# Kernel tuning notes

Hardware: AMD Instinct MI355X
Metric: run time of the kernel (lower is better)

The kernel has to match this reference:

```python
import jax, jax.numpy as jnp
import numpy as np

B, C, N, K = 2, 128, 8192, 16
DL = 128  # dim_L; Fourier half-dim = 64; mlp hidden = 32


def setup_inputs() -> dict:
    key = jax.random.key(0)
    ks = jax.random.split(key, 16)
    s = 0.05
    return {
        "x": jax.random.normal(ks[0], (B, C, N, 1), jnp.float32),
        "coords": jax.random.normal(ks[1], (B, N, 4), jnp.float32),
        "idx": jax.random.randint(ks[2], (B, N, K), 0, N, jnp.int64),
        "B_gauss": jax.random.normal(ks[3], (4, DL // 2), jnp.float32),
        "W1": jax.random.normal(ks[4], (DL, DL // 4), jnp.float32) * s,
        "b1": jax.random.normal(ks[5], (DL // 4,), jnp.float32) * s,
        "W2": jax.random.normal(ks[6], (DL // 4, C), jnp.float32) * s,
        "b2": jax.random.normal(ks[7], (C,), jnp.float32) * s,
        "Wq": jax.random.normal(ks[8], (C, C), jnp.float32) * s,
        "bq": jax.random.normal(ks[9], (C,), jnp.float32) * s,
        "Wk": jax.random.normal(ks[10], (C, C), jnp.float32) * s,
        "bk": jax.random.normal(ks[11], (C,), jnp.float32) * s,
        "Wv": jax.random.normal(ks[12], (C, C), jnp.float32) * s,
        "bv": jax.random.normal(ks[13], (C,), jnp.float32) * s,
        "Wo": jax.random.normal(ks[14], (C, C), jnp.float32) * s,
        "bo": jax.random.normal(ks[15], (C,), jnp.float32) * s,
    }


def reference(x, coords, idx, B_gauss, W1, b1, W2, b2, Wq, bq, Wk, bk, Wv, bv, Wo, bo):
    xs = x[..., 0]  # [B, C, N]
    # gather neighbor coords/features via KNN idx (vmapped over batch)
    nb_coords = jax.vmap(lambda c, i: c[i])(coords, idx)          # [B, N, K, 4]
    nb_feats = jax.vmap(lambda f, i: f[:, i])(xs, idx)            # [B, C, N, K]
    delta_p = nb_coords - coords[:, :, None, :]                   # [B, N, K, 4]
    # random-Fourier geometric embedding
    proj = jnp.matmul(delta_p, B_gauss)                           # [B, N, K, DL/2]
    two_pi = 2.0 * jnp.pi
    E_freq = jnp.concatenate([jnp.sin(two_pi * proj), jnp.cos(two_pi * proj)], axis=-1)
    h = jax.nn.relu(E_freq @ W1 + b1) @ W2 + b2                   # [B, N, K, C]
    E_geo = jnp.transpose(h, (0, 3, 1, 2))                        # [B, C, N, K]
    # 1x1 conv projections == channel matmuls (PyTorch conv weight acts as out<-in)
    Q = jnp.einsum('oc,bcn->bon', Wq, xs) + bq[None, :, None]     # [B, C, N]
    KV_in = nb_feats + E_geo                                      # [B, C, N, K]
    Kt = jnp.einsum('oc,bcnk->bonk', Wk, KV_in) + bk[None, :, None, None]
    Vt = jnp.einsum('oc,bcnk->bonk', Wv, KV_in) + bv[None, :, None, None]
    # local dot-product attention over K neighbors
    attn = jnp.sum(Q[..., None] * Kt, axis=1, keepdims=True) / jnp.sqrt(jnp.float32(C))
    attn = jax.nn.softmax(attn, axis=-1)                          # [B, 1, N, K]
    out = jnp.sum(attn * Vt, axis=-1, keepdims=True)              # [B, C, N, 1]
    out = jnp.einsum('oc,bcnk->bonk', Wo, out) + bo[None, :, None, None]
    return out
```

## Files before the change

kernel.cpp:

```cpp
#include <hip/hip_runtime.h>


using u16 = unsigned short;
using u32 = unsigned int;
using u64 = unsigned long long;

typedef short bf16x8 __attribute__((ext_vector_type(8)));
typedef float f32x4  __attribute__((ext_vector_type(4)));

__device__ __forceinline__ float bl(u32 u) { return __uint_as_float(u << 16); }
__device__ __forceinline__ float bh(u32 u) { return __uint_as_float(u & 0xffff0000u); }
__device__ __forceinline__ float b2f(u16 u) { return __uint_as_float(((u32)u) << 16); }
__device__ __forceinline__ u16 f2b(float f) {
    u32 u = __float_as_uint(f);
    u32 r = u + 0x7fffu + ((u >> 16) & 1u);
    return (u16)(r >> 16);
}
__device__ __forceinline__ float dot8(uint4 wv, const float* xp) {
    float4 a = *(const float4*)xp;
    float4 b = *(const float4*)(xp + 4);
    return bl(wv.x)*a.x + bh(wv.x)*a.y + bl(wv.y)*a.z + bh(wv.y)*a.w
         + bl(wv.z)*b.x + bh(wv.z)*b.y + bl(wv.w)*b.z + bh(wv.w)*b.w;
}
__device__ __forceinline__ u64 pack4(float a, float b, float c, float d) {
    return (u64)f2b(a) | ((u64)f2b(b) << 16) | ((u64)f2b(c) << 32) | ((u64)f2b(d) << 48);
}

__device__ __forceinline__ int fidxA(int m, int c) {
    return (((m >> 4)*4 + (c >> 5))*64 + ((c >> 3) & 3)*16 + (m & 15))*8 + (c & 7);
}

__global__ void __launch_bounds__(512)
k_prep(const float* __restrict__ Wq, const float* __restrict__ bq,
       const float* __restrict__ Wk, const float* __restrict__ bk,
       const float* __restrict__ Wv, const float* __restrict__ bv,
       const float* __restrict__ Wo, const float* __restrict__ bo,
       const float* __restrict__ W1, const float* __restrict__ W2,
       u16* __restrict__ Afrag, u16* __restrict__ Wovfrag,
       u16* __restrict__ W1frag, u16* __restrict__ W2frag,
       u16* __restrict__ W2Tfrag,
       float* __restrict__ bA, float* __restrict__ su,
       float* __restrict__ bov, float* __restrict__ d0)
{
    const int blk = blockIdx.x, tid = threadIdx.x;
    const int i = tid & 127, p = tid >> 7;

    if (blk < 128) {
        __shared__ float sWk[128], sWo[128];
        __shared__ float s_pA[4][128], s_pV[4][128];
        if (tid < 128) sWk[tid] = Wk[tid*128 + blk];
        else if (tid < 256) sWo[tid-128] = Wo[blk*128 + (tid-128)];
        __syncthreads();
        float accA = 0.f, accV = 0.f;
        #pragma unroll 8
        for (int o = p*32; o < p*32 + 32; ++o) {
            accA += sWk[o] * Wq[o*128 + i];
            accV += sWo[o] * Wv[o*128 + i];
        }
        s_pA[p][i] = accA; s_pV[p][i] = accV;
        __syncthreads();
        if (tid < 128) {
            float v = s_pA[0][tid] + s_pA[1][tid] + s_pA[2][tid] + s_pA[3][tid];
            Afrag[fidxA(blk, tid)] = f2b(v);
        } else if (tid < 256) {
            int ii = tid - 128;
            float v = s_pV[0][ii] + s_pV[1][ii] + s_pV[2][ii] + s_pV[3][ii];
            Wovfrag[fidxA(blk, ii)] = f2b(v);
        }
    } else if (blk == 128) {
        __shared__ float s_r[3][4][128];
        float a1 = 0.f, a2 = 0.f, a3 = 0.f;
        #pragma unroll 8
        for (int o = p*32; o < p*32 + 32; ++o) {
            a1 += Wk[o*128 + i] * bq[o];
            a2 += Wq[o*128 + i] * bk[o];
            a3 += Wo[i*128 + o] * bv[o];
        }
        s_r[0][p][i] = a1; s_r[1][p][i] = a2; s_r[2][p][i] = a3;
        __syncthreads();
        if (tid < 128) {
            bA[tid] = s_r[0][0][tid] + s_r[0][1][tid] + s_r[0][2][tid] + s_r[0][3][tid];
        } else if (tid < 256) {
            int ii = tid - 128;
            su[ii] = s_r[1][0][ii] + s_r[1][1][ii] + s_r[1][2][ii] + s_r[1][3][ii];
        } else if (tid < 384) {
            int ii = tid - 256;
            bov[ii] = s_r[2][0][ii] + s_r[2][1][ii] + s_r[2][2][ii] + s_r[2][3][ii] + bo[ii];
        } else if (tid < 448) {
            int l = tid - 384;
            float part = bq[l]*bk[l] + bq[l+64]*bk[l+64];
            part += __shfl_xor(part, 1);
            part += __shfl_xor(part, 2);
            part += __shfl_xor(part, 4);
            part += __shfl_xor(part, 8);
            part += __shfl_xor(part, 16);
            part += __shfl_xor(part, 32);
            if (l == 0) *d0 = part;
        }
    } else {
        for (int e = tid; e < 4096; e += 512) {
            int ii = e & 127, r2 = e >> 7;
            {
                int nt = r2 >> 4, lmm = r2 & 15;
                int ks = ii >> 5, q = (ii >> 3) & 3, j = ii & 7;
                W1frag[((nt*4 + ks)*64 + q*16 + lmm)*8 + j] = f2b(W1[ii*32 + r2]);
            }
            {
                int mt = r2 >> 4, lmm = r2 & 15;
                int ks = ii >> 5, q = (ii >> 3) & 3, j = ii & 7;
                W2frag[((mt*4 + ks)*64 + q*16 + lmm)*8 + j] = f2b(W2[r2*128 + ii]);
            }
            {
                int mt = ii >> 4, lmm = ii & 15;
                int q = r2 >> 3, j = r2 & 7;
                W2Tfrag[(mt*64 + q*16 + lmm)*8 + j] = f2b(W2[r2*128 + ii]);
            }
        }
    }
}

__global__ void k_tr(const float* __restrict__ x, u16* __restrict__ xT)
{
    __shared__ u16 tile[32][33];
    const int blk = blockIdx.x;
    const int b  = blk >> 10;
    const int ct = (blk >> 8) & 3;
    const int nt = blk & 255;
    const int tx = threadIdx.x & 31, ty = threadIdx.x >> 5;
    const size_t xb = (size_t)b * 128 * 8192;
    #pragma unroll
    for (int j = 0; j < 4; ++j) {
        int c = ct*32 + ty + j*8;
        tile[ty + j*8][tx] = f2b(x[xb + (size_t)c * 8192 + (size_t)(nt*32 + tx)]);
    }
    __syncthreads();
    #pragma unroll
    for (int j = 0; j < 4; ++j) {
        int n = nt*32 + ty + j*8;
        xT[xb + (size_t)n * 128 + (size_t)(ct*32 + tx)] = tile[tx][ty + j*8];
    }
}

__global__ void __launch_bounds__(512)
k_main(const u16* __restrict__ xT, const float* __restrict__ coords,
       const int* __restrict__ idx, const float* __restrict__ Bg,
       const float* __restrict__ b1g, const float* __restrict__ b2g,
       const u16* __restrict__ Afrag, const u16* __restrict__ Wovfrag,
       const u16* __restrict__ W1frag, const u16* __restrict__ W2frag,
       const u16* __restrict__ W2Tfrag,
       const float* __restrict__ bAg, const float* __restrict__ sug,
       const float* __restrict__ bovg, const float* __restrict__ d0g,
       float* __restrict__ out)
{
    __shared__ __align__(16) u16   buf[256][136];
    __shared__ __align__(16) u16   sH[256][40];
    __shared__ __align__(16) u16   s_qkb[16][136];
    __shared__ __align__(16) u16   s_gb[16][40];
    __shared__ __align__(16) u16   s_wtb[16][136];
    __shared__ __align__(16) float s_xb[16][132];
    __shared__ __align__(16) float s_del[256][4];
    __shared__ float s_sc[16][17];
    __shared__ float s_attn[16][17];
    __shared__ u16   sHbar[32][18];
    __shared__ float s_e0[16];
    __shared__ __align__(16) float s_b2[128], s_su[128];
    __shared__ float s_bA[128], s_bov[128], s_b1[32];
    __shared__ __align__(16) float sBgT[64][4];
    __shared__ int s_idx[256];

    const int tid = threadIdx.x;
    const int w = tid >> 6, l = tid & 63, lm = l & 15, lq = l >> 4;
    const int g0 = blockIdx.x * 16;
    const int bsel = g0 >> 13;
    const int n0 = g0 & 8191;
    const size_t bbase = ((size_t)bsel) << 13;
    const float inv_sqrtC = 0.08838834764831845f;

    if (tid < 128) {
        s_bA[tid] = bAg[tid]; s_su[tid] = sug[tid];
        s_bov[tid] = bovg[tid]; s_b2[tid] = b2g[tid];
    } else if (tid < 160) {
        s_b1[tid-128] = b1g[tid-128];
    } else if (tid >= 256) {
        int q = tid - 256;
        sBgT[q >> 2][q & 3] = Bg[(q & 3)*64 + (q >> 2)];
    }
    const float c_d0 = *d0g;

    if (tid < 256) {
        int j = idx[(size_t)g0*16 + tid];
        s_idx[tid] = j;
        float4 cj = *(const float4*)&coords[(size_t)(bbase + j)*4];
        float4 cn = *(const float4*)&coords[(size_t)(g0 + (tid >> 4))*4];
        *(float4*)s_del[tid] = make_float4(cj.x-cn.x, cj.y-cn.y, cj.z-cn.z, cj.w-cn.w);
    }
    f32x4 accq = {0.f, 0.f, 0.f, 0.f};
    {
        const bf16x8* Af = (const bf16x8*)Afrag;
        #pragma unroll
        for (int ks = 0; ks < 4; ++ks) {
            bf16x8 a = Af[(w*4 + ks)*64 + l];
            bf16x8 bfr = *(const bf16x8*)&xT[(((size_t)(g0 + lm)) << 7) + ks*32 + lq*8];
            accq = __builtin_amdgcn_mfma_f32_16x16x32_bf16(a, bfr, accq, 0, 0, 0);
        }
    }
    __syncthreads();

    {
        int c0 = w*16 + lq*4;
        *(u64*)&s_qkb[lm][c0] = pack4(accq[0] + s_bA[c0],   accq[1] + s_bA[c0+1],
                                      accq[2] + s_bA[c0+2], accq[3] + s_bA[c0+3]);
    }
    __syncthreads();

    {
        const int row = tid >> 1, ch0 = (tid & 1)*8;
        const size_t rbase = ((size_t)(bbase + s_idx[row])) << 7;
        #pragma unroll
        for (int cc = 0; cc < 8; ++cc) {
            int chunk = ch0 + cc;
            *(uint4*)&buf[row][chunk*8] = *(const uint4*)&xT[rbase + chunk*8];
        }
    }
    {
        const bf16x8* W1f = (const bf16x8*)W1frag;
        bf16x8 w1f[2][4];
        #pragma unroll
        for (int nt = 0; nt < 2; ++nt)
            #pragma unroll
            for (int ks = 0; ks < 4; ++ks) w1f[nt][ks] = W1f[(nt*4 + ks)*64 + l];
        float4 bgc[2][8];
        #pragma unroll
        for (int ksp = 0; ksp < 2; ++ksp)
            #pragma unroll
            for (int j = 0; j < 8; ++j)
                bgc[ksp][j] = *(const float4*)sBgT[ksp*32 + lq*8 + j];
        #pragma unroll
        for (int mi = 0; mi < 2; ++mi) {
            const int mt = w*2 + mi;
            float4 d = *(const float4*)s_del[mt*16 + lm];
            bf16x8 ea[4];
            #pragma unroll
            for (int ksp = 0; ksp < 2; ++ksp) {
                #pragma unroll
                for (int jp = 0; jp < 4; ++jp) {
                    float4 ga = bgc[ksp][jp*2], gb = bgc[ksp][jp*2+1];
                    float p0 = d.x*ga.x + d.y*ga.y + d.z*ga.z + d.w*ga.w;
                    float p1 = d.x*gb.x + d.y*gb.y + d.z*gb.z + d.w*gb.w;
                    p0 -= floorf(p0); p1 -= floorf(p1);
                    ((u32*)&ea[ksp])[jp]   = (u32)f2b(__builtin_amdgcn_sinf(p0))
                                           | ((u32)f2b(__builtin_amdgcn_sinf(p1)) << 16);
                    ((u32*)&ea[ksp+2])[jp] = (u32)f2b(__builtin_amdgcn_cosf(p0))
                                           | ((u32)f2b(__builtin_amdgcn_cosf(p1)) << 16);
                }
            }
            f32x4 acch[2] = {{0.f,0.f,0.f,0.f},{0.f,0.f,0.f,0.f}};
            #pragma unroll
            for (int ks = 0; ks < 4; ++ks) {
                acch[0] = __builtin_amdgcn_mfma_f32_16x16x32_bf16(ea[ks], w1f[0][ks], acch[0], 0,0,0);
                acch[1] = __builtin_amdgcn_mfma_f32_16x16x32_bf16(ea[ks], w1f[1][ks], acch[1], 0,0,0);
            }
            #pragma unroll
            for (int nt = 0; nt < 2; ++nt) {
                float b1v = s_b1[nt*16 + lm];
                #pragma unroll
                for (int r = 0; r < 4; ++r)
                    sH[mt*16 + lq*4 + r][nt*16 + lm] = f2b(fmaxf(acch[nt][r] + b1v, 0.f));
            }
        }
    }
    if (w < 2) {
        const bf16x8* W2f = (const bf16x8*)W2frag;
        f32x4 accg = {0.f,0.f,0.f,0.f};
        #pragma unroll
        for (int ks = 0; ks < 4; ++ks) {
            bf16x8 a = W2f[(w*4 + ks)*64 + l];
            bf16x8 bv = *(const bf16x8*)&s_qkb[lm][ks*32 + lq*8];
            accg = __builtin_amdgcn_mfma_f32_16x16x32_bf16(a, bv, accg, 0, 0, 0);
        }
        int m0 = w*16 + lq*4;
        *(u64*)&s_gb[lm][m0] = pack4(accg[0], accg[1], accg[2], accg[3]);
    } else if (w < 4) {
        int t = tid - 128, n = t >> 3, sub = t & 7, c0 = sub*16;
        uint4 q0 = *(const uint4*)&s_qkb[n][c0];
        uint4 q1 = *(const uint4*)&s_qkb[n][c0+8];
        uint4 x0 = *(const uint4*)&xT[(((size_t)(g0 + n)) << 7) + c0];
        uint4 x1 = *(const uint4*)&xT[(((size_t)(g0 + n)) << 7) + c0 + 8];
        float part = dot8(q0, &s_b2[c0]) + dot8(q1, &s_b2[c0+8])
                   + dot8(x0, &s_su[c0]) + dot8(x1, &s_su[c0+8]);
        part += __shfl_xor(part, 1);
        part += __shfl_xor(part, 2);
        part += __shfl_xor(part, 4);
        if (sub == 0) s_e0[n] = part + c_d0;
    }
    __syncthreads();

    {
        bf16x8 bq4[5];
        #pragma unroll
        for (int ks = 0; ks < 4; ++ks) bq4[ks] = *(const bf16x8*)&s_qkb[lm][ks*32 + lq*8];
        bq4[4] = *(const bf16x8*)&s_gb[lm][lq*8];
        #pragma unroll
        for (int mi = 0; mi < 2; ++mi) {
            const int mt = w*2 + mi;
            f32x4 acc = {0.f,0.f,0.f,0.f};
            #pragma unroll
            for (int ks = 0; ks < 4; ++ks) {
                bf16x8 a = *(const bf16x8*)&buf[mt*16 + lm][ks*32 + lq*8];
                acc = __builtin_amdgcn_mfma_f32_16x16x32_bf16(a, bq4[ks], acc, 0, 0, 0);
            }
            {
                bf16x8 a = *(const bf16x8*)&sH[mt*16 + lm][lq*8];
                acc = __builtin_amdgcn_mfma_f32_16x16x32_bf16(a, bq4[4], acc, 0, 0, 0);
            }
            if (lm == mt) {
                #pragma unroll
                for (int r = 0; r < 4; ++r) s_sc[mt][lq*4 + r] = acc[r];
            }
        }
    }
    __syncthreads();

    if (tid < 256) {
        int n = tid >> 4, k = tid & 15;
        float s = (s_sc[n][k] + s_e0[n]) * inv_sqrtC;
        float mx = s;
        mx = fmaxf(mx, __shfl_xor(mx, 1, 16));
        mx = fmaxf(mx, __shfl_xor(mx, 2, 16));
        mx = fmaxf(mx, __shfl_xor(mx, 4, 16));
        mx = fmaxf(mx, __shfl_xor(mx, 8, 16));
        float ex = __expf(s - mx);
        float sm = ex;
        sm += __shfl_xor(sm, 1, 16);
        sm += __shfl_xor(sm, 2, 16);
        sm += __shfl_xor(sm, 4, 16);
        sm += __shfl_xor(sm, 8, 16);
        s_attn[n][k] = ex / sm;
    }
    __syncthreads();

    {
        int n = tid >> 5, cs = tid & 31, c0 = cs*4;
        float a0[16];
        #pragma unroll
        for (int k = 0; k < 16; ++k) a0[k] = s_attn[n][k];
        float4 facc = *(const float4*)&s_b2[c0];
        #pragma unroll
        for (int k = 0; k < 16; ++k) {
            uint2 v = *(const uint2*)&buf[n*16 + k][c0];
            facc.x += a0[k]*bl(v.x); facc.y += a0[k]*bh(v.x);
            facc.z += a0[k]*bl(v.y); facc.w += a0[k]*bh(v.y);
        }
        *(float4*)&s_xb[n][c0] = facc;
        int m = tid & 31;
        float hacc = 0.f;
        #pragma unroll
        for (int k = 0; k < 16; ++k) hacc += a0[k] * b2f(sH[n*16 + k][m]);
        sHbar[m][n] = f2b(hacc);
    }
    __syncthreads();

    {
        const bf16x8* W2Tf = (const bf16x8*)W2Tfrag;
        bf16x8 a = W2Tf[w*64 + l];
        bf16x8 bv;
        #pragma unroll
        for (int j = 0; j < 8; ++j) bv[j] = (short)sHbar[lq*8 + j][lm];
        f32x4 accw = {0.f,0.f,0.f,0.f};
        accw = __builtin_amdgcn_mfma_f32_16x16x32_bf16(a, bv, accw, 0, 0, 0);
        int c0 = w*16 + lq*4;
        float4 xb4 = *(const float4*)&s_xb[lm][c0];
        *(u64*)&s_wtb[lm][c0] = pack4(xb4.x + accw[0], xb4.y + accw[1],
                                      xb4.z + accw[2], xb4.w + accw[3]);
    }
    __syncthreads();

    {
        const bf16x8* Wvf = (const bf16x8*)Wovfrag;
        f32x4 acco = {0.f,0.f,0.f,0.f};
        #pragma unroll
        for (int ks = 0; ks < 4; ++ks) {
            bf16x8 a = Wvf[(w*4 + ks)*64 + l];
            bf16x8 bv = *(const bf16x8*)&s_wtb[lm][ks*32 + lq*8];
            acco = __builtin_amdgcn_mfma_f32_16x16x32_bf16(a, bv, acco, 0, 0, 0);
        }
        #pragma unroll
        for (int r = 0; r < 4; ++r) {
            int o = w*16 + lq*4 + r;
            out[(((size_t)(bsel*128 + o)) << 13) + n0 + lm] = acco[r] + s_bov[o];
        }
    }
}

extern "C" void kernel_launch(void* const* d_in, const int* in_sizes, int n_in,
                              void* d_out, int out_size, void* d_ws, size_t ws_size,
                              hipStream_t stream)
{
    const float* x      = (const float*)d_in[0];
    const float* coords = (const float*)d_in[1];
    const int*   idx    = (const int*)d_in[2];
    const float* Bg     = (const float*)d_in[3];
    const float* W1     = (const float*)d_in[4];
    const float* b1     = (const float*)d_in[5];
    const float* W2     = (const float*)d_in[6];
    const float* b2     = (const float*)d_in[7];
    const float* Wq     = (const float*)d_in[8];
    const float* bq     = (const float*)d_in[9];
    const float* Wk     = (const float*)d_in[10];
    const float* bk     = (const float*)d_in[11];
    const float* Wv     = (const float*)d_in[12];
    const float* bv     = (const float*)d_in[13];
    const float* Wo     = (const float*)d_in[14];
    const float* bo     = (const float*)d_in[15];
    float* out = (float*)d_out;

    char* ws = (char*)d_ws;
    u16*   Afrag   = (u16*)(ws);
    u16*   Wovfrag = (u16*)(ws + 32768);
    u16*   W1frag  = (u16*)(ws + 65536);
    u16*   W2frag  = (u16*)(ws + 73728);
    u16*   W2Tfrag = (u16*)(ws + 81920);
    float* bA      = (float*)(ws + 90112);
    float* su      = (float*)(ws + 90624);
    float* bov     = (float*)(ws + 91136);
    float* d0      = (float*)(ws + 91648);
    u16*   xT      = (u16*)(ws + 94208);

    k_prep<<<130, 512, 0, stream>>>(Wq, bq, Wk, bk, Wv, bv, Wo, bo, W1, W2,
                                    Afrag, Wovfrag, W1frag, W2frag, W2Tfrag,
                                    bA, su, bov, d0);
    k_tr<<<2048, 256, 0, stream>>>(x, xT);
    k_main<<<1024, 512, 0, stream>>>(xT, coords, idx, Bg, b1, b2,
                                     Afrag, Wovfrag, W1frag, W2frag, W2Tfrag,
                                     bA, su, bov, d0, out);
}
```

Before: 137.1 us.

## Halve main-kernel tile, drop neighbor LDS staging, merge prep and transpose kernels

The main kernel now handles 8 points per block with 256 threads instead of 16 points with 512 threads, and uses launch bounds of 5 blocks per CU. This cuts shared memory sharply and should raise occupancy. Gathered neighbor features are no longer staged in the 256x136 LDS buffer but read straight from global xT inside the MFMA and aggregation loops. The weight-prep and transpose kernels are merged into one launch to save a kernel boundary. The trade-off is that half the MFMA lanes (lm>=8) do wasted work, and global gathers are repeated, relying on the cache.

```diff
diff --git a/kernel.cpp b/kernel.cpp
--- a/kernel.cpp
+++ b/kernel.cpp
@@ -25,26 +25,49 @@
 __device__ __forceinline__ u64 pack4(float a, float b, float c, float d) {
     return (u64)f2b(a) | ((u64)f2b(b) << 16) | ((u64)f2b(c) << 32) | ((u64)f2b(d) << 48);
 }
-
 __device__ __forceinline__ int fidxA(int m, int c) {
     return (((m >> 4)*4 + (c >> 5))*64 + ((c >> 3) & 3)*16 + (m & 15))*8 + (c & 7);
 }
 
 __global__ void __launch_bounds__(512)
-k_prep(const float* __restrict__ Wq, const float* __restrict__ bq,
-       const float* __restrict__ Wk, const float* __restrict__ bk,
-       const float* __restrict__ Wv, const float* __restrict__ bv,
-       const float* __restrict__ Wo, const float* __restrict__ bo,
-       const float* __restrict__ W1, const float* __restrict__ W2,
-       u16* __restrict__ Afrag, u16* __restrict__ Wovfrag,
-       u16* __restrict__ W1frag, u16* __restrict__ W2frag,
-       u16* __restrict__ W2Tfrag,
-       float* __restrict__ bA, float* __restrict__ su,
-       float* __restrict__ bov, float* __restrict__ d0)
+k_pt(const float* __restrict__ x,
+     const float* __restrict__ Wq, const float* __restrict__ bq,
+     const float* __restrict__ Wk, const float* __restrict__ bk,
+     const float* __restrict__ Wv, const float* __restrict__ bv,
+     const float* __restrict__ Wo, const float* __restrict__ bo,
+     const float* __restrict__ W1, const float* __restrict__ W2,
+     u16* __restrict__ Afrag, u16* __restrict__ Wovfrag,
+     u16* __restrict__ W1frag, u16* __restrict__ W2frag,
+     u16* __restrict__ W2Tfrag,
+     float* __restrict__ bA, float* __restrict__ su,
+     float* __restrict__ bov, float* __restrict__ d0,
+     u16* __restrict__ xT)
 {
     const int blk = blockIdx.x, tid = threadIdx.x;
+
+    if (blk >= 130) {
+        __shared__ u16 tile[32][33];
+        const int blk2 = blk - 130;
+        const int b  = blk2 >> 10;
+        const int ct = (blk2 >> 8) & 3;
+        const int nt = blk2 & 255;
+        const int tx = tid & 31, ty = tid >> 5;
+        const size_t xb = (size_t)b * 128 * 8192;
+        #pragma unroll
+        for (int j = 0; j < 2; ++j) {
+            int c = ct*32 + ty + j*16;
+            tile[ty + j*16][tx] = f2b(x[xb + (size_t)c * 8192 + (size_t)(nt*32 + tx)]);
+        }
+        __syncthreads();
+        #pragma unroll
+        for (int j = 0; j < 2; ++j) {
+            int n = nt*32 + ty + j*16;
+            xT[xb + (size_t)n * 128 + (size_t)(ct*32 + tx)] = tile[tx][ty + j*16];
+        }
+        return;
+    }
+
     const int i = tid & 127, p = tid >> 7;
-
     if (blk < 128) {
         __shared__ float sWk[128], sWo[128];
         __shared__ float s_pA[4][128], s_pV[4][128];
@@ -119,29 +142,7 @@
     }
 }
 
-__global__ void k_tr(const float* __restrict__ x, u16* __restrict__ xT)
-{
-    __shared__ u16 tile[32][33];
-    const int blk = blockIdx.x;
-    const int b  = blk >> 10;
-    const int ct = (blk >> 8) & 3;
-    const int nt = blk & 255;
-    const int tx = threadIdx.x & 31, ty = threadIdx.x >> 5;
-    const size_t xb = (size_t)b * 128 * 8192;
-    #pragma unroll
-    for (int j = 0; j < 4; ++j) {
-        int c = ct*32 + ty + j*8;
-        tile[ty + j*8][tx] = f2b(x[xb + (size_t)c * 8192 + (size_t)(nt*32 + tx)]);
-    }
-    __syncthreads();
-    #pragma unroll
-    for (int j = 0; j < 4; ++j) {
-        int n = nt*32 + ty + j*8;
-        xT[xb + (size_t)n * 128 + (size_t)(ct*32 + tx)] = tile[tx][ty + j*8];
-    }
-}
-
-__global__ void __launch_bounds__(512)
+__global__ void __launch_bounds__(256, 5)
 k_main(const u16* __restrict__ xT, const float* __restrict__ coords,
        const int* __restrict__ idx, const float* __restrict__ Bg,
        const float* __restrict__ b1g, const float* __restrict__ b2g,
@@ -152,25 +153,24 @@
        const float* __restrict__ bovg, const float* __restrict__ d0g,
        float* __restrict__ out)
 {
-    __shared__ __align__(16) u16   buf[256][136];
-    __shared__ __align__(16) u16   sH[256][40];
-    __shared__ __align__(16) u16   s_qkb[16][136];
-    __shared__ __align__(16) u16   s_gb[16][40];
-    __shared__ __align__(16) u16   s_wtb[16][136];
-    __shared__ __align__(16) float s_xb[16][132];
-    __shared__ __align__(16) float s_del[256][4];
-    __shared__ float s_sc[16][17];
-    __shared__ float s_attn[16][17];
-    __shared__ u16   sHbar[32][18];
-    __shared__ float s_e0[16];
+    __shared__ __align__(16) u16   sH[128][40];
+    __shared__ __align__(16) u16   s_qkb[8][136];
+    __shared__ __align__(16) u16   s_gb[8][40];
+    __shared__ __align__(16) u16   s_wtb[8][136];
+    __shared__ __align__(16) float s_xb[8][132];
+    __shared__ __align__(16) float s_del[128][4];
+    __shared__ float s_sc[8][17];
+    __shared__ float s_attn[8][17];
+    __shared__ u16   sHbar[32][12];
+    __shared__ float s_e0[8];
     __shared__ __align__(16) float s_b2[128], s_su[128];
     __shared__ float s_bA[128], s_bov[128], s_b1[32];
     __shared__ __align__(16) float sBgT[64][4];
-    __shared__ int s_idx[256];
+    __shared__ int s_idx[128];
 
     const int tid = threadIdx.x;
-    const int w = tid >> 6, l = tid & 63, lm = l & 15, lq = l >> 4;
-    const int g0 = blockIdx.x * 16;
+    const int w = tid >> 6, l = tid & 63, lm = l & 15, lq = l >> 4, lmm = lm & 7;
+    const int g0 = blockIdx.x * 8;
     const int bsel = g0 >> 13;
     const int n0 = g0 & 8191;
     const size_t bbase = ((size_t)bsel) << 13;
@@ -181,47 +181,46 @@
         s_bov[tid] = bovg[tid]; s_b2[tid] = b2g[tid];
     } else if (tid < 160) {
         s_b1[tid-128] = b1g[tid-128];
-    } else if (tid >= 256) {
-        int q = tid - 256;
-        sBgT[q >> 2][q & 3] = Bg[(q & 3)*64 + (q >> 2)];
-    }
+    }
+    sBgT[tid >> 2][tid & 3] = Bg[(tid & 3)*64 + (tid >> 2)];
     const float c_d0 = *d0g;
 
-    if (tid < 256) {
+    if (tid < 128) {
         int j = idx[(size_t)g0*16 + tid];
         s_idx[tid] = j;
         float4 cj = *(const float4*)&coords[(size_t)(bbase + j)*4];
         float4 cn = *(const float4*)&coords[(size_t)(g0 + (tid >> 4))*4];
         *(float4*)s_del[tid] = make_float4(cj.x-cn.x, cj.y-cn.y, cj.z-cn.z, cj.w-cn.w);
     }
-    f32x4 accq = {0.f, 0.f, 0.f, 0.f};
+    f32x4 accq[2] = {{0.f,0.f,0.f,0.f},{0.f,0.f,0.f,0.f}};
     {
         const bf16x8* Af = (const bf16x8*)Afrag;
-        #pragma unroll
-        for (int ks = 0; ks < 4; ++ks) {
-            bf16x8 a = Af[(w*4 + ks)*64 + l];
-            bf16x8 bfr = *(const bf16x8*)&xT[(((size_t)(g0 + lm)) << 7) + ks*32 + lq*8];
-            accq = __builtin_amdgcn_mfma_f32_16x16x32_bf16(a, bfr, accq, 0, 0, 0);
-        }
-    }
-    __syncthreads();
-
-    {
-        int c0 = w*16 + lq*4;
-        *(u64*)&s_qkb[lm][c0] = pack4(accq[0] + s_bA[c0],   accq[1] + s_bA[c0+1],
-                                      accq[2] + s_bA[c0+2], accq[3] + s_bA[c0+3]);
-    }
-    __syncthreads();
-
-    {
-        const int row = tid >> 1, ch0 = (tid & 1)*8;
-        const size_t rbase = ((size_t)(bbase + s_idx[row])) << 7;
-        #pragma unroll
-        for (int cc = 0; cc < 8; ++cc) {
-            int chunk = ch0 + cc;
-            *(uint4*)&buf[row][chunk*8] = *(const uint4*)&xT[rbase + chunk*8];
-        }
-    }
+        bf16x8 bfr[4];
+        #pragma unroll
+        for (int ks = 0; ks < 4; ++ks)
+            bfr[ks] = *(const bf16x8*)&xT[(((size_t)(g0 + lmm)) << 7) + ks*32 + lq*8];
+        #pragma unroll
+        for (int mi = 0; mi < 2; ++mi) {
+            const int ct = w*2 + mi;
+            #pragma unroll
+            for (int ks = 0; ks < 4; ++ks) {
+                bf16x8 a = Af[(ct*4 + ks)*64 + l];
+                accq[mi] = __builtin_amdgcn_mfma_f32_16x16x32_bf16(a, bfr[ks], accq[mi], 0, 0, 0);
+            }
+        }
+    }
+    __syncthreads();
+
+    if (lm < 8) {
+        #pragma unroll
+        for (int mi = 0; mi < 2; ++mi) {
+            int c0 = (w*2 + mi)*16 + lq*4;
+            *(u64*)&s_qkb[lm][c0] = pack4(accq[mi][0] + s_bA[c0],   accq[mi][1] + s_bA[c0+1],
+                                          accq[mi][2] + s_bA[c0+2], accq[mi][3] + s_bA[c0+3]);
+        }
+    }
+    __syncthreads();
+
     {
         const bf16x8* W1f = (const bf16x8*)W1frag;
         bf16x8 w1f[2][4];
@@ -229,12 +228,6 @@
         for (int nt = 0; nt < 2; ++nt)
             #pragma unroll
             for (int ks = 0; ks < 4; ++ks) w1f[nt][ks] = W1f[(nt*4 + ks)*64 + l];
-        float4 bgc[2][8];
-        #pragma unroll
-        for (int ksp = 0; ksp < 2; ++ksp)
-            #pragma unroll
-            for (int j = 0; j < 8; ++j)
-                bgc[ksp][j] = *(const float4*)sBgT[ksp*32 + lq*8 + j];
         #pragma unroll
         for (int mi = 0; mi < 2; ++mi) {
             const int mt = w*2 + mi;
@@ -244,7 +237,9 @@
             for (int ksp = 0; ksp < 2; ++ksp) {
                 #pragma unroll
                 for (int jp = 0; jp < 4; ++jp) {
-                    float4 ga = bgc[ksp][jp*2], gb = bgc[ksp][jp*2+1];
+                    int f = ksp*32 + lq*8 + jp*2;
+                    float4 ga = *(const float4*)sBgT[f];
+                    float4 gb = *(const float4*)sBgT[f+1];
                     float p0 = d.x*ga.x + d.y*ga.y + d.z*ga.z + d.w*ga.w;
                     float p1 = d.x*gb.x + d.y*gb.y + d.z*gb.z + d.w*gb.w;
                     p0 -= floorf(p0); p1 -= floorf(p1);
@@ -275,38 +270,44 @@
         #pragma unroll
         for (int ks = 0; ks < 4; ++ks) {
             bf16x8 a = W2f[(w*4 + ks)*64 + l];
-            bf16x8 bv = *(const bf16x8*)&s_qkb[lm][ks*32 + lq*8];
+            bf16x8 bv = *(const bf16x8*)&s_qkb[lmm][ks*32 + lq*8];
             accg = __builtin_amdgcn_mfma_f32_16x16x32_bf16(a, bv, accg, 0, 0, 0);
         }
-        int m0 = w*16 + lq*4;
-        *(u64*)&s_gb[lm][m0] = pack4(accg[0], accg[1], accg[2], accg[3]);
-    } else if (w < 4) {
-        int t = tid - 128, n = t >> 3, sub = t & 7, c0 = sub*16;
-        uint4 q0 = *(const uint4*)&s_qkb[n][c0];
-        uint4 q1 = *(const uint4*)&s_qkb[n][c0+8];
-        uint4 x0 = *(const uint4*)&xT[(((size_t)(g0 + n)) << 7) + c0];
-        uint4 x1 = *(const uint4*)&xT[(((size_t)(g0 + n)) << 7) + c0 + 8];
-        float part = dot8(q0, &s_b2[c0]) + dot8(q1, &s_b2[c0+8])
-                   + dot8(x0, &s_su[c0]) + dot8(x1, &s_su[c0+8]);
-        part += __shfl_xor(part, 1);
-        part += __shfl_xor(part, 2);
-        part += __shfl_xor(part, 4);
-        if (sub == 0) s_e0[n] = part + c_d0;
+        if (lm < 8) {
+            int m0 = w*16 + lq*4;
+            *(u64*)&s_gb[lm][m0] = pack4(accg[0], accg[1], accg[2], accg[3]);
+        }
+    } else {
+        int t = tid - 128;
+        if (t < 64) {
+            int n = t >> 3, sub = t & 7, c0 = sub*16;
+            uint4 q0 = *(const uint4*)&s_qkb[n][c0];
+            uint4 q1 = *(const uint4*)&s_qkb[n][c0+8];
+            uint4 x0 = *(const uint4*)&xT[(((size_t)(g0 + n)) << 7) + c0];
+            uint4 x1 = *(const uint4*)&xT[(((size_t)(g0 + n)) << 7) + c0 + 8];
+            float part = dot8(q0, &s_b2[c0]) + dot8(q1, &s_b2[c0+8])
+                       + dot8(x0, &s_su[c0]) + dot8(x1, &s_su[c0+8]);
+            part += __shfl_xor(part, 1);
+            part += __shfl_xor(part, 2);
+            part += __shfl_xor(part, 4);
+            if (sub == 0) s_e0[n] = part + c_d0;
+        }
     }
     __syncthreads();
 
     {
         bf16x8 bq4[5];
         #pragma unroll
-        for (int ks = 0; ks < 4; ++ks) bq4[ks] = *(const bf16x8*)&s_qkb[lm][ks*32 + lq*8];
-        bq4[4] = *(const bf16x8*)&s_gb[lm][lq*8];
+        for (int ks = 0; ks < 4; ++ks) bq4[ks] = *(const bf16x8*)&s_qkb[lmm][ks*32 + lq*8];
+        bq4[4] = *(const bf16x8*)&s_gb[lmm][lq*8];
         #pragma unroll
         for (int mi = 0; mi < 2; ++mi) {
             const int mt = w*2 + mi;
+            const size_t rb = ((size_t)(bbase + s_idx[mt*16 + lm])) << 7;
             f32x4 acc = {0.f,0.f,0.f,0.f};
             #pragma unroll
             for (int ks = 0; ks < 4; ++ks) {
-                bf16x8 a = *(const bf16x8*)&buf[mt*16 + lm][ks*32 + lq*8];
+                bf16x8 a = *(const bf16x8*)&xT[rb + ks*32 + lq*8];
                 acc = __builtin_amdgcn_mfma_f32_16x16x32_bf16(a, bq4[ks], acc, 0, 0, 0);
             }
             {
@@ -321,7 +322,7 @@
     }
     __syncthreads();
 
-    if (tid < 256) {
+    if (tid < 128) {
         int n = tid >> 4, k = tid & 15;
         float s = (s_sc[n][k] + s_e0[n]) * inv_sqrtC;
         float mx = s;
@@ -347,12 +348,12 @@
         float4 facc = *(const float4*)&s_b2[c0];
         #pragma unroll
         for (int k = 0; k < 16; ++k) {
-            uint2 v = *(const uint2*)&buf[n*16 + k][c0];
+            uint2 v = *(const uint2*)&xT[(((size_t)(bbase + s_idx[n*16 + k])) << 7) + c0];
             facc.x += a0[k]*bl(v.x); facc.y += a0[k]*bh(v.x);
             facc.z += a0[k]*bl(v.y); facc.w += a0[k]*bh(v.y);
         }
         *(float4*)&s_xb[n][c0] = facc;
-        int m = tid & 31;
+        int m = cs;
         float hacc = 0.f;
         #pragma unroll
         for (int k = 0; k < 16; ++k) hacc += a0[k] * b2f(sH[n*16 + k][m]);
@@ -362,32 +363,46 @@
 
     {
         const bf16x8* W2Tf = (const bf16x8*)W2Tfrag;
-        bf16x8 a = W2Tf[w*64 + l];
         bf16x8 bv;
         #pragma unroll
-        for (int j = 0; j < 8; ++j) bv[j] = (short)sHbar[lq*8 + j][lm];
-        f32x4 accw = {0.f,0.f,0.f,0.f};
-        accw = __builtin_amdgcn_mfma_f32_16x16x32_bf16(a, bv, accw, 0, 0, 0);
-        int c0 = w*16 + lq*4;
-        float4 xb4 = *(const float4*)&s_xb[lm][c0];
-        *(u64*)&s_wtb[lm][c0] = pack4(xb4.x + accw[0], xb4.y + accw[1],
-                                      xb4.z + accw[2], xb4.w + accw[3]);
+        for (int j = 0; j < 8; ++j) bv[j] = (short)sHbar[lq*8 + j][lmm];
+        #pragma unroll
+        for (int mi = 0; mi < 2; ++mi) {
+            const int mt = w*2 + mi;
+            bf16x8 a = W2Tf[mt*64 + l];
+            f32x4 accw = {0.f,0.f,0.f,0.f};
+            accw = __builtin_amdgcn_mfma_f32_16x16x32_bf16(a, bv, accw, 0, 0, 0);
+            if (lm < 8) {
+                int c0 = mt*16 + lq*4;
+                float4 xb4 = *(const float4*)&s_xb[lm][c0];
+                *(u64*)&s_wtb[lm][c0] = pack4(xb4.x + accw[0], xb4.y + accw[1],
+                                              xb4.z + accw[2], xb4.w + accw[3]);
+            }
+        }
     }
     __syncthreads();
 
     {
         const bf16x8* Wvf = (const bf16x8*)Wovfrag;
-        f32x4 acco = {0.f,0.f,0.f,0.f};
-        #pragma unroll
-        for (int ks = 0; ks < 4; ++ks) {
-            bf16x8 a = Wvf[(w*4 + ks)*64 + l];
-            bf16x8 bv = *(const bf16x8*)&s_wtb[lm][ks*32 + lq*8];
-            acco = __builtin_amdgcn_mfma_f32_16x16x32_bf16(a, bv, acco, 0, 0, 0);
-        }
-        #pragma unroll
-        for (int r = 0; r < 4; ++r) {
-            int o = w*16 + lq*4 + r;
-            out[(((size_t)(bsel*128 + o)) << 13) + n0 + lm] = acco[r] + s_bov[o];
+        bf16x8 bv[4];
+        #pragma unroll
+        for (int ks = 0; ks < 4; ++ks) bv[ks] = *(const bf16x8*)&s_wtb[lmm][ks*32 + lq*8];
+        #pragma unroll
+        for (int mi = 0; mi < 2; ++mi) {
+            const int ct = w*2 + mi;
+            f32x4 acco = {0.f,0.f,0.f,0.f};
+            #pragma unroll
+            for (int ks = 0; ks < 4; ++ks) {
+                bf16x8 a = Wvf[(ct*4 + ks)*64 + l];
+                acco = __builtin_amdgcn_mfma_f32_16x16x32_bf16(a, bv[ks], acco, 0, 0, 0);
+            }
+            if (lm < 8) {
+                #pragma unroll
+                for (int r = 0; r < 4; ++r) {
+                    int o = ct*16 + lq*4 + r;
+                    out[(((size_t)(bsel*128 + o)) << 13) + n0 + lm] = acco[r] + s_bov[o];
+                }
+            }
         }
     }
 }
@@ -426,11 +441,10 @@
     float* d0      = (float*)(ws + 91648);
     u16*   xT      = (u16*)(ws + 94208);
 
-    k_prep<<<130, 512, 0, stream>>>(Wq, bq, Wk, bk, Wv, bv, Wo, bo, W1, W2,
-                                    Afrag, Wovfrag, W1frag, W2frag, W2Tfrag,
-                                    bA, su, bov, d0);
-    k_tr<<<2048, 256, 0, stream>>>(x, xT);
-    k_main<<<1024, 512, 0, stream>>>(xT, coords, idx, Bg, b1, b2,
+    k_pt<<<2178, 512, 0, stream>>>(x, Wq, bq, Wk, bk, Wv, bv, Wo, bo, W1, W2,
+                                   Afrag, Wovfrag, W1frag, W2frag, W2Tfrag,
+                                   bA, su, bov, d0, xT);
+    k_main<<<2048, 256, 0, stream>>>(xT, coords, idx, Bg, b1, b2,
                                      Afrag, Wovfrag, W1frag, W2frag, W2Tfrag,
                                      bA, su, bov, d0, out);
 }
```

Measured after the change: 192.0 us. 40.0% more time.
